# Kernel optimization log

Hardware: AMD Instinct MI355X
Metric: run time of the kernel (lower is better)

The kernel has to match this reference:

```python
import jax, jax.numpy as jnp
import numpy as np

N = 50000
NEIGH = 32
D_IN = 128
D_OUT = 128

def setup_inputs() -> dict:
    key = jax.random.key(0)
    k1, k2, k3, k4 = jax.random.split(key, 4)
    self_vecs = jax.random.normal(k1, (N, D_IN), dtype=jnp.float32)
    neigh_vecs = jax.random.normal(k2, (N * NEIGH, D_IN), dtype=jnp.float32)
    weight = jax.random.normal(k3, (D_IN, D_OUT), dtype=jnp.float32) * (1.0 / np.sqrt(D_IN))
    bias = jax.random.normal(k4, (D_OUT,), dtype=jnp.float32) * 0.01
    return {"self_vecs": self_vecs, "neigh_vecs": neigh_vecs, "neigh_num": NEIGH,
            "weight": weight, "bias": bias}

def reference(self_vecs, neigh_vecs, neigh_num, weight, bias):
    # self_h: [N, 1, F], neigh_h: [N, neigh_num, F]
    self_h = jnp.matmul(self_vecs, weight)[:, None, :]
    neigh_h = jnp.matmul(neigh_vecs, weight).reshape(-1, neigh_num, weight.shape[1])
    # concat along neighbor axis then mean == mean of (neigh_num+1) rows
    out = jnp.mean(jnp.concatenate([self_h, neigh_h], axis=1), axis=1)
    return out + bias
```

## Files before the change

kernel.cpp:

```cpp
#include <hip/hip_runtime.h>


typedef float f32x4 __attribute__((ext_vector_type(4)));

constexpr int D        = 128;
constexpr int NEIGH    = 32;
constexpr int WAVES    = 8;
constexpr int THREADS  = WAVES * 64;
constexpr int NPW      = 4;
constexpr int NPB      = WAVES * NPW;

__global__ __launch_bounds__(THREADS, 4)
void sparse_layer_fused(const float* __restrict__ self_vecs,
                        const float* __restrict__ neigh_vecs,
                        const float* __restrict__ weight,
                        const float* __restrict__ bias,
                        float* __restrict__ out, int n_nodes)
{
    __shared__ float w_lds[D * D];
    __shared__ float agg_lds[NPB][D];

    {
        const f32x4* w4 = reinterpret_cast<const f32x4*>(weight);
        f32x4*       wl = reinterpret_cast<f32x4*>(w_lds);
        #pragma unroll
        for (int i = 0; i < (D * D / 4) / THREADS; ++i)
            wl[threadIdx.x + i * THREADS] = w4[threadIdx.x + i * THREADS];
    }
    __syncthreads();

    const int wave = threadIdx.x >> 6;
    const int lane = threadIdx.x & 63;
    const int half = lane >> 5;
    const int c4   = lane & 31;

    const int  lA = wave * NPW + half;
    const int  lB = lA + 2;
    const long nA = (long)blockIdx.x * NPB + lA;
    const long nB = nA + 2;
    const bool vA = nA < n_nodes;
    const bool vB = nB < n_nodes;

    const f32x4* s4 = reinterpret_cast<const f32x4*>(self_vecs);
    const f32x4* g4 = reinterpret_cast<const f32x4*>(neigh_vecs);

    constexpr float inv = 1.0f / (NEIGH + 1);
    f32x4 aA = (f32x4)0.0f;
    f32x4 aB = (f32x4)0.0f;

    if (vB) {
        aA = s4[nA * (D / 4) + c4];
        aB = s4[nB * (D / 4) + c4];
        const f32x4* pA = g4 + nA * (long)NEIGH * (D / 4) + c4;
        const f32x4* pB = g4 + nB * (long)NEIGH * (D / 4) + c4;
        #pragma unroll 8
        for (int r = 0; r < NEIGH; ++r) {
            f32x4 u = __builtin_nontemporal_load(&pA[(long)r * (D / 4)]);
            f32x4 v = __builtin_nontemporal_load(&pB[(long)r * (D / 4)]);
            aA += u;
            aB += v;
        }
    } else if (vA) {
        aA = s4[nA * (D / 4) + c4];
        const f32x4* pA = g4 + nA * (long)NEIGH * (D / 4) + c4;
        #pragma unroll 8
        for (int r = 0; r < NEIGH; ++r) {
            f32x4 u = __builtin_nontemporal_load(&pA[(long)r * (D / 4)]);
            aA += u;
        }
    }
    if (vA) reinterpret_cast<f32x4*>(agg_lds[lA])[c4] = aA * inv;
    if (vB) reinterpret_cast<f32x4*>(agg_lds[lB])[c4] = aB * inv;

    f32x4 oA = (f32x4)0.0f;
    f32x4 oB = (f32x4)0.0f;
    const f32x4* wl  = reinterpret_cast<const f32x4*>(w_lds);
    const f32x4* arA = reinterpret_cast<const f32x4*>(agg_lds[lA]);
    const f32x4* arB = reinterpret_cast<const f32x4*>(agg_lds[lB]);
    #pragma unroll 4
    for (int k4 = 0; k4 < D / 4; ++k4) {
        f32x4 a0 = arA[k4];
        f32x4 a1 = arB[k4];
        f32x4 w0 = wl[(4*k4 + 0) * (D/4) + c4];
        f32x4 w1 = wl[(4*k4 + 1) * (D/4) + c4];
        f32x4 w2 = wl[(4*k4 + 2) * (D/4) + c4];
        f32x4 w3 = wl[(4*k4 + 3) * (D/4) + c4];
        oA += a0.x * w0;  oA += a0.y * w1;  oA += a0.z * w2;  oA += a0.w * w3;
        oB += a1.x * w0;  oB += a1.y * w1;  oB += a1.z * w2;  oB += a1.w * w3;
    }
    const f32x4 b = reinterpret_cast<const f32x4*>(bias)[c4];
    if (vA) reinterpret_cast<f32x4*>(out)[nA * (D / 4) + c4] = oA + b;
    if (vB) reinterpret_cast<f32x4*>(out)[nB * (D / 4) + c4] = oB + b;
}

extern "C" void kernel_launch(void* const* d_in, const int* in_sizes, int n_in,
                              void* d_out, int out_size, void* d_ws, size_t ws_size,
                              hipStream_t stream) {
    const float* self_vecs  = (const float*)d_in[0];
    const float* neigh_vecs = (const float*)d_in[1];
    const float* weight     = (const float*)d_in[3];
    const float* bias       = (const float*)d_in[4];
    float*       out        = (float*)d_out;

    const int n_nodes = in_sizes[0] / D;
    const int blocks  = (n_nodes + NPB - 1) / NPB;
    hipLaunchKernelGGL(sparse_layer_fused, dim3(blocks), dim3(THREADS), 0, stream,
                       self_vecs, neigh_vecs, weight, bias, out, n_nodes);
}
```

Before: 173.4 us.

## Make kernel persistent and overlap next tile's neighbor loads with current GEMV

Launches a fixed grid of 512 blocks that loop over node tiles, so the weight matrix is loaded into LDS once per block rather than once per tile. Inside the loop, the neighbor rows for the next tile are loaded and summed while the current tile's LDS-based matrix-vector product runs, aiming to hide HBM latency behind compute. Self-vector loads are also made nontemporal. The risks are fewer waves available to hide memory latency, a longer serial dependency per block, and the agg_lds overwrite relying on intra-wave ordering with no barrier.

Result: slower. 186.0 us (+7.3%).

```diff
diff --git a/kernel.cpp b/kernel.cpp
--- a/kernel.cpp
+++ b/kernel.cpp
@@ -3,29 +3,31 @@
 
 typedef float f32x4 __attribute__((ext_vector_type(4)));
 
-constexpr int D        = 128;
-constexpr int NEIGH    = 32;
-constexpr int WAVES    = 8;
-constexpr int THREADS  = WAVES * 64;
-constexpr int NPW      = 4;
-constexpr int NPB      = WAVES * NPW;
+constexpr int D       = 128;
+constexpr int D4      = D / 4;
+constexpr int NEIGH   = 32;
+constexpr int WAVES   = 8;
+constexpr int THREADS = WAVES * 64;
+constexpr int NPW     = 4;
+constexpr int NPB     = WAVES * NPW;
+constexpr int GRID    = 512;
 
 __global__ __launch_bounds__(THREADS, 4)
-void sparse_layer_fused(const float* __restrict__ self_vecs,
-                        const float* __restrict__ neigh_vecs,
-                        const float* __restrict__ weight,
-                        const float* __restrict__ bias,
-                        float* __restrict__ out, int n_nodes)
+void sparse_layer_pipe(const float* __restrict__ self_vecs,
+                       const float* __restrict__ neigh_vecs,
+                       const float* __restrict__ weight,
+                       const float* __restrict__ bias,
+                       float* __restrict__ out, int n_nodes)
 {
     __shared__ float w_lds[D * D];
     __shared__ float agg_lds[NPB][D];
 
     {
         const f32x4* w4 = reinterpret_cast<const f32x4*>(weight);
-        f32x4*       wl = reinterpret_cast<f32x4*>(w_lds);
+        f32x4*       wp = reinterpret_cast<f32x4*>(w_lds);
         #pragma unroll
         for (int i = 0; i < (D * D / 4) / THREADS; ++i)
-            wl[threadIdx.x + i * THREADS] = w4[threadIdx.x + i * THREADS];
+            wp[threadIdx.x + i * THREADS] = w4[threadIdx.x + i * THREADS];
     }
     __syncthreads();
 
@@ -34,63 +36,84 @@
     const int half = lane >> 5;
     const int c4   = lane & 31;
 
-    const int  lA = wave * NPW + half;
-    const int  lB = lA + 2;
-    const long nA = (long)blockIdx.x * NPB + lA;
-    const long nB = nA + 2;
-    const bool vA = nA < n_nodes;
-    const bool vB = nB < n_nodes;
+    const int lA = wave * NPW + half;
+    const int lB = lA + 2;
 
     const f32x4* s4 = reinterpret_cast<const f32x4*>(self_vecs);
     const f32x4* g4 = reinterpret_cast<const f32x4*>(neigh_vecs);
+    const f32x4* wl = reinterpret_cast<const f32x4*>(w_lds);
+    f32x4* arA = reinterpret_cast<f32x4*>(agg_lds[lA]);
+    f32x4* arB = reinterpret_cast<f32x4*>(agg_lds[lB]);
+    const f32x4 bv = reinterpret_cast<const f32x4*>(bias)[c4];
+    constexpr float inv = 1.0f / (NEIGH + 1);
 
-    constexpr float inv = 1.0f / (NEIGH + 1);
-    f32x4 aA = (f32x4)0.0f;
-    f32x4 aB = (f32x4)0.0f;
+    const int n_tiles = (n_nodes + NPB - 1) / NPB;
 
-    if (vB) {
-        aA = s4[nA * (D / 4) + c4];
-        aB = s4[nB * (D / 4) + c4];
-        const f32x4* pA = g4 + nA * (long)NEIGH * (D / 4) + c4;
-        const f32x4* pB = g4 + nB * (long)NEIGH * (D / 4) + c4;
-        #pragma unroll 8
-        for (int r = 0; r < NEIGH; ++r) {
-            f32x4 u = __builtin_nontemporal_load(&pA[(long)r * (D / 4)]);
-            f32x4 v = __builtin_nontemporal_load(&pB[(long)r * (D / 4)]);
-            aA += u;
-            aB += v;
+    int t = blockIdx.x;
+    if (t >= n_tiles) return;
+
+    {
+        const long nA = (long)t * NPB + lA, nB = nA + 2;
+        const bool vA = nA < n_nodes, vB = nB < n_nodes;
+        f32x4 aA = (f32x4)0.0f, aB = (f32x4)0.0f;
+        const f32x4* pA = g4 + nA * (long)NEIGH * D4 + c4;
+        const f32x4* pB = g4 + nB * (long)NEIGH * D4 + c4;
+        if (vB) {
+            aA = __builtin_nontemporal_load(&s4[nA * D4 + c4]);
+            aB = __builtin_nontemporal_load(&s4[nB * D4 + c4]);
+            #pragma unroll 8
+            for (int r = 0; r < NEIGH; ++r) {
+                aA += __builtin_nontemporal_load(&pA[r * D4]);
+                aB += __builtin_nontemporal_load(&pB[r * D4]);
+            }
+        } else if (vA) {
+            aA = __builtin_nontemporal_load(&s4[nA * D4 + c4]);
+            #pragma unroll 8
+            for (int r = 0; r < NEIGH; ++r)
+                aA += __builtin_nontemporal_load(&pA[r * D4]);
         }
-    } else if (vA) {
-        aA = s4[nA * (D / 4) + c4];
-        const f32x4* pA = g4 + nA * (long)NEIGH * (D / 4) + c4;
-        #pragma unroll 8
-        for (int r = 0; r < NEIGH; ++r) {
-            f32x4 u = __builtin_nontemporal_load(&pA[(long)r * (D / 4)]);
-            aA += u;
+        if (vA) arA[c4] = aA * inv;
+        if (vB) arB[c4] = aB * inv;
+    }
+
+    for (; t < n_tiles; t += GRID) {
+        const int  tn  = t + GRID;
+        const long mA  = (long)tn * NPB + lA, mB = mA + 2;
+        const bool wAv = (tn < n_tiles) && (mA < n_nodes);
+        const bool wBv = (tn < n_tiles) && (mB < n_nodes);
+        const f32x4* qA = g4 + mA * (long)NEIGH * D4 + c4;
+        const f32x4* qB = g4 + mB * (long)NEIGH * D4 + c4;
+        f32x4 nxA = (f32x4)0.0f, nxB = (f32x4)0.0f;
+        if (wAv) nxA = __builtin_nontemporal_load(&s4[mA * D4 + c4]);
+        if (wBv) nxB = __builtin_nontemporal_load(&s4[mB * D4 + c4]);
+
+        f32x4 oA = (f32x4)0.0f, oB = (f32x4)0.0f;
+
+        #pragma unroll 4
+        for (int k4 = 0; k4 < D4; ++k4) {
+            if (wBv) {
+                nxA += __builtin_nontemporal_load(&qA[k4 * D4]);
+                nxB += __builtin_nontemporal_load(&qB[k4 * D4]);
+            } else if (wAv) {
+                nxA += __builtin_nontemporal_load(&qA[k4 * D4]);
+            }
+            f32x4 a0 = arA[k4];
+            f32x4 a1 = arB[k4];
+            f32x4 w0 = wl[(4 * k4 + 0) * D4 + c4];
+            f32x4 w1 = wl[(4 * k4 + 1) * D4 + c4];
+            f32x4 w2 = wl[(4 * k4 + 2) * D4 + c4];
+            f32x4 w3 = wl[(4 * k4 + 3) * D4 + c4];
+            oA += a0.x * w0;  oA += a0.y * w1;  oA += a0.z * w2;  oA += a0.w * w3;
+            oB += a1.x * w0;  oB += a1.y * w1;  oB += a1.z * w2;  oB += a1.w * w3;
         }
+
+        const long nA = (long)t * NPB + lA, nB = nA + 2;
+        if (nA < n_nodes) reinterpret_cast<f32x4*>(out)[nA * D4 + c4] = oA + bv;
+        if (nB < n_nodes) reinterpret_cast<f32x4*>(out)[nB * D4 + c4] = oB + bv;
+
+        if (wAv) arA[c4] = nxA * inv;
+        if (wBv) arB[c4] = nxB * inv;
     }
-    if (vA) reinterpret_cast<f32x4*>(agg_lds[lA])[c4] = aA * inv;
-    if (vB) reinterpret_cast<f32x4*>(agg_lds[lB])[c4] = aB * inv;
-
-    f32x4 oA = (f32x4)0.0f;
-    f32x4 oB = (f32x4)0.0f;
-    const f32x4* wl  = reinterpret_cast<const f32x4*>(w_lds);
-    const f32x4* arA = reinterpret_cast<const f32x4*>(agg_lds[lA]);
-    const f32x4* arB = reinterpret_cast<const f32x4*>(agg_lds[lB]);
-    #pragma unroll 4
-    for (int k4 = 0; k4 < D / 4; ++k4) {
-        f32x4 a0 = arA[k4];
-        f32x4 a1 = arB[k4];
-        f32x4 w0 = wl[(4*k4 + 0) * (D/4) + c4];
-        f32x4 w1 = wl[(4*k4 + 1) * (D/4) + c4];
-        f32x4 w2 = wl[(4*k4 + 2) * (D/4) + c4];
-        f32x4 w3 = wl[(4*k4 + 3) * (D/4) + c4];
-        oA += a0.x * w0;  oA += a0.y * w1;  oA += a0.z * w2;  oA += a0.w * w3;
-        oB += a1.x * w0;  oB += a1.y * w1;  oB += a1.z * w2;  oB += a1.w * w3;
-    }
-    const f32x4 b = reinterpret_cast<const f32x4*>(bias)[c4];
-    if (vA) reinterpret_cast<f32x4*>(out)[nA * (D / 4) + c4] = oA + b;
-    if (vB) reinterpret_cast<f32x4*>(out)[nB * (D / 4) + c4] = oB + b;
 }
 
 extern "C" void kernel_launch(void* const* d_in, const int* in_sizes, int n_in,
@@ -103,7 +126,8 @@
     float*       out        = (float*)d_out;
 
     const int n_nodes = in_sizes[0] / D;
-    const int blocks  = (n_nodes + NPB - 1) / NPB;
-    hipLaunchKernelGGL(sparse_layer_fused, dim3(blocks), dim3(THREADS), 0, stream,
+    const int n_tiles = (n_nodes + NPB - 1) / NPB;
+    const int blocks  = n_tiles < GRID ? n_tiles : GRID;
+    hipLaunchKernelGGL(sparse_layer_pipe, dim3(blocks), dim3(THREADS), 0, stream,
                        self_vecs, neigh_vecs, weight, bias, out, n_nodes);
 }
```
